# Kernel optimization log

Measured on AMD Instinct MI355X. Metric: run time of the kernel, lower is better.

Reference implementation:

```python
import jax, jax.numpy as jnp
import numpy as np

N_WAY = 5
K_SHOT = 5
SEQ = 196          # patch tokens per image (ViT-S/16 @ 224)
TEMP = 0.0510310363  # similarity temperature ~ 1/sqrt(384)
LR = 0.1
OPT_STEPS = 15


def _normalize(emb):
    # [B, S, D] -> [B*S, D], rows L2-normalized with 1e-8 floor (matches torch.max(norm, 1e-8))
    v = emb.reshape(-1, emb.shape[-1])
    n = jnp.linalg.norm(v, axis=1, keepdims=True)
    return v / jnp.maximum(n, 1e-8)


def _block_mask():
    # block_diag of (SEQ x SEQ) blocks of -100 for each of the n_way*k_shot support images
    return jnp.kron(jnp.eye(N_WAY * K_SHOT, dtype=jnp.float32),
                    jnp.ones((SEQ, SEQ), jnp.float32)) * (-100.0)


def _predict(sup, qry, v, mask):
    # sup: [n_way*k_shot, S, D], qry: [Qb, Qs, D], v: [n_way*k_shot*S]
    S = sup.shape[1]
    Qb, Qs = qry.shape[0], qry.shape[1]
    C = _normalize(sup) @ _normalize(qry).T           # [Ls, Qb*Qs] cosine sims
    if mask is not None:
        C = C + mask
    pred = C + v[:, None]
    pred = pred.reshape(N_WAY, K_SHOT * S, Qb, Qs)
    pred = pred.transpose(0, 1, 3, 2).reshape(N_WAY, K_SHOT * S * Qs, Qb)
    pred = pred / TEMP
    pred = jax.scipy.special.logsumexp(pred, axis=1)  # [n_way, Qb]
    return pred.T                                     # [Qb, n_way]


def _optimize_v(sup_key, sup_query, labels, mask):
    # online SGD on the patch-embedding importance vector v (starts at zero)
    Ls = N_WAY * K_SHOT * sup_key.shape[1]
    B = sup_query.shape[0]

    def loss(v):
        p = _predict(sup_key, sup_query, v, mask)  # [B, n_way]
        logp = jax.nn.log_softmax(p, axis=1)
        return -jnp.mean(logp[jnp.arange(B), labels])

    def step(v, _):
        return v - LR * jax.grad(loss)(v), None

    v, _ = jax.lax.scan(step, jnp.zeros((Ls,), jnp.float32), None, length=OPT_STEPS)
    return v


def setup_inputs() -> dict:
    key = jax.random.key(0)
    k1, k2, k3, k4 = jax.random.split(key, 4)
    return {
        "support_emb_key": jax.random.normal(k1, (N_WAY * K_SHOT, SEQ, 384), jnp.float32),
        "support_emb_query": jax.random.normal(k2, (N_WAY * K_SHOT, SEQ, 384), jnp.float32),
        "query_emb": jax.random.normal(k3, (75, SEQ, 384), jnp.float32),
        "support_labels": jax.random.randint(k4, (N_WAY * K_SHOT,), 0, N_WAY, dtype=jnp.int32),
    }


def reference(support_emb_key, support_emb_query, query_emb, support_labels):
    mask = _block_mask()
    v = _optimize_v(support_emb_key, support_emb_query, support_labels, mask)
    return _predict(support_emb_key, query_emb, v, None)  # [75, n_way]
```

## Files before the change

### kernel.cpp

```cpp
#include <hip/hip_runtime.h>
#include <hip/hip_bf16.h>

#define NW 5
#define KS 5
#define SEQ 196
#define DIM 384
#define NSUP 25
#define NQRY 75
#define NIMG 100
#define LSUP 4900
#define LSUP_PAD 4992
#define QROWS 208
#define BLOCK_W 980
#define OPT_STEPS 15
#define MTILES 39

static constexpr float TEMP_F = 0.0510310363f;
static constexpr float INV_T  = 1.0f / TEMP_F;
static constexpr float LR_F   = 0.1f;

typedef short v8s __attribute__((ext_vector_type(8)));
typedef float v4f __attribute__((ext_vector_type(4)));

__device__ inline unsigned short f2bf(float x) {
    unsigned int u = __float_as_uint(x);
    u += 0x7fffu + ((u >> 16) & 1u);
    return (unsigned short)(u >> 16);
}

__global__ __launch_bounds__(128) void norm_k(const float* __restrict__ src,
                                              unsigned short* __restrict__ dst) {
    int row = blockIdx.x;
    unsigned short* out = dst + (size_t)row * DIM;
    int t = threadIdx.x;
    if (row >= LSUP) {
        out[t] = 0; out[t + 128] = 0; out[t + 256] = 0;
        return;
    }
    const float* in = src + (size_t)row * DIM;
    float x0 = in[t], x1 = in[t + 128], x2 = in[t + 256];
    float s = x0 * x0 + x1 * x1 + x2 * x2;
    #pragma unroll
    for (int off = 32; off; off >>= 1) s += __shfl_down(s, off);
    __shared__ float wsum[2];
    if ((t & 63) == 0) wsum[t >> 6] = s;
    __syncthreads();
    float sc = INV_T / fmaxf(sqrtf(wsum[0] + wsum[1]), 1e-8f);
    out[t]       = f2bf(x0 * sc);
    out[t + 128] = f2bf(x1 * sc);
    out[t + 256] = f2bf(x2 * sc);
}

__global__ __launch_bounds__(128) void norm_q(const float* __restrict__ supq,
                                              const float* __restrict__ qry,
                                              unsigned short* __restrict__ dst) {
    int r = blockIdx.x;
    int img = blockIdx.y;
    unsigned short* out = dst + ((size_t)img * QROWS + r) * DIM;
    int t = threadIdx.x;
    if (r >= SEQ) {
        out[t] = 0; out[t + 128] = 0; out[t + 256] = 0;
        return;
    }
    const float* in = (img < NSUP)
        ? supq + ((size_t)img * SEQ + r) * DIM
        : qry  + ((size_t)(img - NSUP) * SEQ + r) * DIM;
    float x0 = in[t], x1 = in[t + 128], x2 = in[t + 256];
    float s = x0 * x0 + x1 * x1 + x2 * x2;
    #pragma unroll
    for (int off = 32; off; off >>= 1) s += __shfl_down(s, off);
    __shared__ float wsum[2];
    if ((t & 63) == 0) wsum[t >> 6] = s;
    __syncthreads();
    float sc = 1.0f / fmaxf(sqrtf(wsum[0] + wsum[1]), 1e-8f);
    out[t]       = f2bf(x0 * sc);
    out[t + 128] = f2bf(x1 * sc);
    out[t + 256] = f2bf(x2 * sc);
}

#define MT  128
#define NTP 208
#define NTT 13
#define KCC 64

__device__ __forceinline__ void gload16(const void* g, void* l) {
    __builtin_amdgcn_global_load_lds(
        (__attribute__((address_space(1))) void*)g,
        (__attribute__((address_space(3))) void*)l, 16, 0, 0);
}

__global__ __launch_bounds__(256, 3) void fused_expsum_mfma(
    const unsigned short* __restrict__ Kb,
    const unsigned short* __restrict__ Qall,
    float* __restrict__ Rall)
{
    __shared__ __align__(16) unsigned short Asm[MT * KCC];
    __shared__ __align__(16) unsigned short Bsm[NTP * KCC];

    int t = threadIdx.x;

    int bid = blockIdx.x;
    int xcd = bid & 7;
    int sub = bid >> 3;
    const int qq = (MTILES * NIMG) >> 3;
    const int rr = (MTILES * NIMG) & 7;
    int L = (xcd < rr ? xcd * (qq + 1) : rr * (qq + 1) + (xcd - rr) * qq) + sub;
    int img = L / MTILES;
    int m_base = (L - img * MTILES) * MT;

    const unsigned short* Qimg = Qall + (size_t)img * (QROWS * DIM);

    int wv = t >> 6;
    int l  = t & 63;
    int lo = l & 15;
    int hi = l >> 4;

    int srow = l >> 3;
    int skp  = (l & 7) ^ srow;
    const unsigned short* aSrc = Kb   + (size_t)(m_base + wv * 32 + srow) * DIM + skp * 8;
    const unsigned short* bSrc = Qimg + (size_t)srow * DIM + skp * 8;

    v4f acc0[NTT], acc1[NTT];
    #pragma unroll
    for (int n = 0; n < NTT; ++n) {
        acc0[n] = (v4f){0.f, 0.f, 0.f, 0.f};
        acc1[n] = (v4f){0.f, 0.f, 0.f, 0.f};
    }

    for (int kb = 0; kb < DIM; kb += KCC) {
        #pragma unroll
        for (int j = 0; j < 4; ++j)
            gload16(aSrc + (size_t)j * 8 * DIM + kb,
                    Asm + (wv * 32 + j * 8) * KCC);
        #pragma unroll
        for (int jj = 0; jj < 7; ++jj) {
            int j = wv + jj * 4;
            if (j < 26)
                gload16(bSrc + (size_t)j * 8 * DIM + kb,
                        Bsm + j * 8 * KCC);
        }
        __syncthreads();

        const unsigned short* Ar0 = Asm + (wv * 32 + lo) * KCC;
        const unsigned short* Br  = Bsm + lo * KCC;
        #pragma unroll
        for (int kk = 0; kk < 2; ++kk) {
            int koff = ((hi + 4 * kk) ^ (lo & 7)) * 8;
            v8s a0 = *(const v8s*)(Ar0 + koff);
            v8s a1 = *(const v8s*)(Ar0 + 16 * KCC + koff);
            #pragma unroll
            for (int n = 0; n < NTT; ++n) {
                v8s bb = *(const v8s*)(Br + n * 16 * KCC + koff);
                acc0[n] = __builtin_amdgcn_mfma_f32_16x16x32_bf16(a0, bb, acc0[n], 0, 0, 0);
                acc1[n] = __builtin_amdgcn_mfma_f32_16x16x32_bf16(a1, bb, acc1[n], 0, 0, 0);
            }
        }
        __syncthreads();
    }

    float s0[4] = {0.f, 0.f, 0.f, 0.f}, s1[4] = {0.f, 0.f, 0.f, 0.f};
    #pragma unroll
    for (int n = 0; n < NTT; ++n) {
        bool ok = (n * 16 + lo) < SEQ;
        #pragma unroll
        for (int j = 0; j < 4; ++j) {
            s0[j] += ok ? __expf(acc0[n][j]) : 0.f;
            s1[j] += ok ? __expf(acc1[n][j]) : 0.f;
        }
    }
    #pragma unroll
    for (int m = 1; m < 16; m <<= 1) {
        #pragma unroll
        for (int j = 0; j < 4; ++j) {
            s0[j] += __shfl_xor(s0[j], m);
            s1[j] += __shfl_xor(s1[j], m);
        }
    }
    if (lo == 0) {
        #pragma unroll
        for (int j = 0; j < 4; ++j) {
            int r0 = m_base + wv * 32 + hi * 4 + j;
            int r1 = r0 + 16;
            if (r0 < LSUP) {
                float o = s0[j];
                if (img < NSUP && (r0 / SEQ) == img) o = 0.f;
                Rall[(size_t)img * LSUP + r0] = o;
            }
            if (r1 < LSUP) {
                float o = s1[j];
                if (img < NSUP && (r1 / SEQ) == img) o = 0.f;
                Rall[(size_t)img * LSUP + r1] = o;
            }
        }
    }
}

__global__ __launch_bounds__(512) void opt_fused(
    const float* __restrict__ Rall,
    const int* __restrict__ labels,
    float* __restrict__ Dbufs,
    float* __restrict__ out,
    int* __restrict__ bar)
{
    __shared__ float cfs[NSUP];
    __shared__ float red[8][NSUP];
    __shared__ float esm[512];

    int blk = blockIdx.x;
    int w = blk >> 1, h = blk & 1;
    int t = threadIdx.x;
    int wave = t >> 6, lane = t & 63;
    bool act = t < 490;
    int ls = w * BLOCK_W + h * 490 + t;

    int gen = 0;
    auto gridbar = [&]() {
        __syncthreads();
        if (t == 0) {
            ++gen;
            __hip_atomic_fetch_add(bar, 1, __ATOMIC_RELEASE, __HIP_MEMORY_SCOPE_AGENT);
            while (__hip_atomic_load(bar, __ATOMIC_ACQUIRE, __HIP_MEMORY_SCOPE_AGENT) < gen * 10) {}
        }
        __syncthreads();
    };

    float Rv[NSUP];
    #pragma unroll
    for (int b = 0; b < NSUP; ++b)
        Rv[b] = act ? Rall[(size_t)b * LSUP + ls] : 0.f;

    float vv = 0.f;
    float e  = 1.f;

    {
        float part[NSUP];
        #pragma unroll
        for (int b = 0; b < NSUP; ++b) part[b] = Rv[b];
        #pragma unroll
        for (int b = 0; b < NSUP; ++b) {
            #pragma unroll
            for (int m = 32; m; m >>= 1) part[b] += __shfl_xor(part[b], m);
        }
        if (lane == 0) {
            #pragma unroll
            for (int b = 0; b < NSUP; ++b) red[wave][b] = part[b];
        }
        __syncthreads();
        if (t < NSUP) {
            float s = 0.f;
            #pragma unroll
            for (int wv2 = 0; wv2 < 8; ++wv2) s += red[wv2][t];
            atomicAdd(&Dbufs[t * 5 + w], s);
        }
    }

    for (int s = 0; s < OPT_STEPS; ++s) {
        gridbar();
        const float* Dp = Dbufs + s * 125;
        if (t < NSUP) {
            int b = t;
            float Dsum = 0.f, Dw = 1.f;
            #pragma unroll
            for (int ww = 0; ww < 5; ++ww) {
                float d = Dp[b * 5 + ww];
                Dsum += d;
                if (ww == w) Dw = d;
            }
            int y = labels[b];
            cfs[b] = ((Dw / Dsum) - (w == y ? 1.f : 0.f)) * (INV_T / 25.f) / Dw;
        }
        __syncthreads();
        float g = 0.f;
        #pragma unroll
        for (int b = 0; b < NSUP; ++b) g += cfs[b] * Rv[b];
        if (act) {
            vv -= LR_F * e * g;
            e = __expf(vv * INV_T);
        }
        __syncthreads();
        if (s + 1 < OPT_STEPS) {
            float part[NSUP];
            #pragma unroll
            for (int b = 0; b < NSUP; ++b) part[b] = e * Rv[b];
            #pragma unroll
            for (int b = 0; b < NSUP; ++b) {
                #pragma unroll
                for (int m = 32; m; m >>= 1) part[b] += __shfl_xor(part[b], m);
            }
            if (lane == 0) {
                #pragma unroll
                for (int b = 0; b < NSUP; ++b) red[wave][b] = part[b];
            }
            __syncthreads();
            if (t < NSUP) {
                float s2 = 0.f;
                #pragma unroll
                for (int wv2 = 0; wv2 < 8; ++wv2) s2 += red[wv2][t];
                atomicAdd(&Dbufs[(s + 1) * 125 + t * 5 + w], s2);
            }
        }
    }

    esm[t] = act ? e : 0.f;
    __syncthreads();
    for (int qb = wave; qb < NQRY; qb += 8) {
        const float* R = Rall + (size_t)(NSUP + qb) * LSUP + w * BLOCK_W + h * 490;
        float p = 0.f;
        for (int i = lane; i < 490; i += 64) p += esm[i] * R[i];
        #pragma unroll
        for (int m = 32; m; m >>= 1) p += __shfl_xor(p, m);
        if (lane == 0) atomicAdd(&out[qb * 5 + w], p);
    }
    gridbar();
    if (blk == 0) {
        for (int i = t; i < NQRY * NW; i += 512) out[i] = logf(out[i]);
    }
}

extern "C" void kernel_launch(void* const* d_in, const int* in_sizes, int n_in,
                              void* d_out, int out_size, void* d_ws, size_t ws_size,
                              hipStream_t stream) {
    const float* sup_key = (const float*)d_in[0];
    const float* sup_qry = (const float*)d_in[1];
    const float* qry     = (const float*)d_in[2];
    const int*   labels  = (const int*)d_in[3];
    float* out = (float*)d_out;

    char* ws = (char*)d_ws;
    size_t off = 0;
    auto take = [&](size_t bytes) {
        char* p = ws + off;
        off = (off + bytes + 255) & ~(size_t)255;
        return p;
    };
    unsigned short* Kb   = (unsigned short*)take((size_t)LSUP_PAD * DIM * 2);
    unsigned short* Qall = (unsigned short*)take((size_t)NIMG * QROWS * DIM * 2);
    float*          Rall = (float*)take((size_t)NIMG * LSUP * 4);
    float*          Dbuf = (float*)take(((size_t)(OPT_STEPS + 1) * 125 + 64) * 4);
    int*            bar  = (int*)(Dbuf + (OPT_STEPS + 1) * 125);

    hipMemsetAsync(Dbuf, 0, ((size_t)(OPT_STEPS + 1) * 125 + 64) * 4, stream);
    hipMemsetAsync(out, 0, (size_t)NQRY * NW * 4, stream);

    norm_k<<<LSUP_PAD, 128, 0, stream>>>(sup_key, Kb);
    norm_q<<<dim3(QROWS, NIMG), 128, 0, stream>>>(sup_qry, qry, Qall);

    fused_expsum_mfma<<<MTILES * NIMG, 256, 0, stream>>>(Kb, Qall, Rall);

    opt_fused<<<10, 512, 0, stream>>>(Rall, labels, Dbuf, out, bar);
}
```

Before: 256.5 us.

## Retile MFMA waves to 64x112, use wave-per-row norms, drop grid barrier

The GEMM kernel now gives each wave a 64-row by 112-column tile instead of 32x208, so each B fragment loaded from LDS feeds four MFMAs rather than two. The two column halves are then combined through shared memory before writing Rall. The norm kernels use one wave per row with a shuffle-only reduction and no __syncthreads. The optimizer kernel runs with 5 blocks of 1024 threads instead of 10. It replaces the atomic grid barrier with per-slot release stores and spin-polling on nonzero values, and the final log is computed directly without atomics. The spin on nonzero values assumes no partial sum is ever exactly zero, and the retiled GEMM uses more accumulator registers.

Result: slower. 326.8 us (+27.4%).

```diff
diff --git a/kernel.cpp b/kernel.cpp
--- a/kernel.cpp
+++ b/kernel.cpp
@@ -28,54 +28,56 @@
     return (unsigned short)(u >> 16);
 }
 
-__global__ __launch_bounds__(128) void norm_k(const float* __restrict__ src,
+__global__ __launch_bounds__(256) void norm_k(const float* __restrict__ src,
                                               unsigned short* __restrict__ dst) {
-    int row = blockIdx.x;
+    int row = blockIdx.x * 4 + (threadIdx.x >> 6);
+    int l = threadIdx.x & 63;
     unsigned short* out = dst + (size_t)row * DIM;
-    int t = threadIdx.x;
     if (row >= LSUP) {
-        out[t] = 0; out[t + 128] = 0; out[t + 256] = 0;
+        #pragma unroll
+        for (int k = 0; k < 6; ++k) out[l + 64 * k] = 0;
         return;
     }
     const float* in = src + (size_t)row * DIM;
-    float x0 = in[t], x1 = in[t + 128], x2 = in[t + 256];
-    float s = x0 * x0 + x1 * x1 + x2 * x2;
-    #pragma unroll
-    for (int off = 32; off; off >>= 1) s += __shfl_down(s, off);
-    __shared__ float wsum[2];
-    if ((t & 63) == 0) wsum[t >> 6] = s;
-    __syncthreads();
-    float sc = INV_T / fmaxf(sqrtf(wsum[0] + wsum[1]), 1e-8f);
-    out[t]       = f2bf(x0 * sc);
-    out[t + 128] = f2bf(x1 * sc);
-    out[t + 256] = f2bf(x2 * sc);
-}
-
-__global__ __launch_bounds__(128) void norm_q(const float* __restrict__ supq,
+    float x[6];
+    #pragma unroll
+    for (int k = 0; k < 6; ++k) x[k] = in[l + 64 * k];
+    float s = 0.f;
+    #pragma unroll
+    for (int k = 0; k < 6; ++k) s += x[k] * x[k];
+    #pragma unroll
+    for (int m = 1; m < 64; m <<= 1) s += __shfl_xor(s, m);
+    float sc = INV_T / fmaxf(sqrtf(s), 1e-8f);
+    #pragma unroll
+    for (int k = 0; k < 6; ++k) out[l + 64 * k] = f2bf(x[k] * sc);
+}
+
+__global__ __launch_bounds__(256) void norm_q(const float* __restrict__ supq,
                                               const float* __restrict__ qry,
                                               unsigned short* __restrict__ dst) {
-    int r = blockIdx.x;
+    int r = blockIdx.x * 4 + (threadIdx.x >> 6);
     int img = blockIdx.y;
+    int l = threadIdx.x & 63;
     unsigned short* out = dst + ((size_t)img * QROWS + r) * DIM;
-    int t = threadIdx.x;
     if (r >= SEQ) {
-        out[t] = 0; out[t + 128] = 0; out[t + 256] = 0;
+        #pragma unroll
+        for (int k = 0; k < 6; ++k) out[l + 64 * k] = 0;
         return;
     }
     const float* in = (img < NSUP)
         ? supq + ((size_t)img * SEQ + r) * DIM
         : qry  + ((size_t)(img - NSUP) * SEQ + r) * DIM;
-    float x0 = in[t], x1 = in[t + 128], x2 = in[t + 256];
-    float s = x0 * x0 + x1 * x1 + x2 * x2;
-    #pragma unroll
-    for (int off = 32; off; off >>= 1) s += __shfl_down(s, off);
-    __shared__ float wsum[2];
-    if ((t & 63) == 0) wsum[t >> 6] = s;
-    __syncthreads();
-    float sc = 1.0f / fmaxf(sqrtf(wsum[0] + wsum[1]), 1e-8f);
-    out[t]       = f2bf(x0 * sc);
-    out[t + 128] = f2bf(x1 * sc);
-    out[t + 256] = f2bf(x2 * sc);
+    float x[6];
+    #pragma unroll
+    for (int k = 0; k < 6; ++k) x[k] = in[l + 64 * k];
+    float s = 0.f;
+    #pragma unroll
+    for (int k = 0; k < 6; ++k) s += x[k] * x[k];
+    #pragma unroll
+    for (int m = 1; m < 64; m <<= 1) s += __shfl_xor(s, m);
+    float sc = 1.0f / fmaxf(sqrtf(s), 1e-8f);
+    #pragma unroll
+    for (int k = 0; k < 6; ++k) out[l + 64 * k] = f2bf(x[k] * sc);
 }
 
 #define MT  128
@@ -114,18 +116,20 @@
     int l  = t & 63;
     int lo = l & 15;
     int hi = l >> 4;
+    int mh = (wv >> 1) * 64;
+    int nh = wv & 1;
 
     int srow = l >> 3;
     int skp  = (l & 7) ^ srow;
     const unsigned short* aSrc = Kb   + (size_t)(m_base + wv * 32 + srow) * DIM + skp * 8;
     const unsigned short* bSrc = Qimg + (size_t)srow * DIM + skp * 8;
 
-    v4f acc0[NTT], acc1[NTT];
-    #pragma unroll
-    for (int n = 0; n < NTT; ++n) {
-        acc0[n] = (v4f){0.f, 0.f, 0.f, 0.f};
-        acc1[n] = (v4f){0.f, 0.f, 0.f, 0.f};
-    }
+    v4f acc[4][7];
+    #pragma unroll
+    for (int m = 0; m < 4; ++m)
+        #pragma unroll
+        for (int n = 0; n < 7; ++n)
+            acc[m][n] = (v4f){0.f, 0.f, 0.f, 0.f};
 
     for (int kb = 0; kb < DIM; kb += KCC) {
         #pragma unroll
@@ -141,101 +145,103 @@
         }
         __syncthreads();
 
-        const unsigned short* Ar0 = Asm + (wv * 32 + lo) * KCC;
-        const unsigned short* Br  = Bsm + lo * KCC;
+        const unsigned short* Ar = Asm + (mh + lo) * KCC;
+        const unsigned short* Br = Bsm + (nh * 112 + lo) * KCC;
         #pragma unroll
         for (int kk = 0; kk < 2; ++kk) {
             int koff = ((hi + 4 * kk) ^ (lo & 7)) * 8;
-            v8s a0 = *(const v8s*)(Ar0 + koff);
-            v8s a1 = *(const v8s*)(Ar0 + 16 * KCC + koff);
-            #pragma unroll
-            for (int n = 0; n < NTT; ++n) {
-                v8s bb = *(const v8s*)(Br + n * 16 * KCC + koff);
-                acc0[n] = __builtin_amdgcn_mfma_f32_16x16x32_bf16(a0, bb, acc0[n], 0, 0, 0);
-                acc1[n] = __builtin_amdgcn_mfma_f32_16x16x32_bf16(a1, bb, acc1[n], 0, 0, 0);
+            v8s a0 = *(const v8s*)(Ar + koff);
+            v8s a1 = *(const v8s*)(Ar + 16 * KCC + koff);
+            v8s a2 = *(const v8s*)(Ar + 32 * KCC + koff);
+            v8s a3 = *(const v8s*)(Ar + 48 * KCC + koff);
+            #pragma unroll
+            for (int n = 0; n < 7; ++n) {
+                if (nh == 0 || n < 6) {
+                    v8s bb = *(const v8s*)(Br + n * 16 * KCC + koff);
+                    acc[0][n] = __builtin_amdgcn_mfma_f32_16x16x32_bf16(a0, bb, acc[0][n], 0, 0, 0);
+                    acc[1][n] = __builtin_amdgcn_mfma_f32_16x16x32_bf16(a1, bb, acc[1][n], 0, 0, 0);
+                    acc[2][n] = __builtin_amdgcn_mfma_f32_16x16x32_bf16(a2, bb, acc[2][n], 0, 0, 0);
+                    acc[3][n] = __builtin_amdgcn_mfma_f32_16x16x32_bf16(a3, bb, acc[3][n], 0, 0, 0);
+                }
             }
         }
         __syncthreads();
     }
 
-    float s0[4] = {0.f, 0.f, 0.f, 0.f}, s1[4] = {0.f, 0.f, 0.f, 0.f};
-    #pragma unroll
-    for (int n = 0; n < NTT; ++n) {
-        bool ok = (n * 16 + lo) < SEQ;
-        #pragma unroll
-        for (int j = 0; j < 4; ++j) {
-            s0[j] += ok ? __expf(acc0[n][j]) : 0.f;
-            s1[j] += ok ? __expf(acc1[n][j]) : 0.f;
-        }
-    }
-    #pragma unroll
-    for (int m = 1; m < 16; m <<= 1) {
-        #pragma unroll
-        for (int j = 0; j < 4; ++j) {
-            s0[j] += __shfl_xor(s0[j], m);
-            s1[j] += __shfl_xor(s1[j], m);
-        }
-    }
+    float s[4][4];
+    #pragma unroll
+    for (int m = 0; m < 4; ++m)
+        #pragma unroll
+        for (int j = 0; j < 4; ++j) s[m][j] = 0.f;
+    #pragma unroll
+    for (int n = 0; n < 7; ++n) {
+        if (nh == 0 || n < 6) {
+            bool ok = ((nh * 7 + n) * 16 + lo) < SEQ;
+            #pragma unroll
+            for (int m = 0; m < 4; ++m)
+                #pragma unroll
+                for (int j = 0; j < 4; ++j)
+                    s[m][j] += ok ? __expf(acc[m][n][j]) : 0.f;
+        }
+    }
+    #pragma unroll
+    for (int mm = 1; mm < 16; mm <<= 1) {
+        #pragma unroll
+        for (int m = 0; m < 4; ++m)
+            #pragma unroll
+            for (int j = 0; j < 4; ++j)
+                s[m][j] += __shfl_xor(s[m][j], mm);
+    }
+    float* rp = (float*)Asm;
     if (lo == 0) {
         #pragma unroll
-        for (int j = 0; j < 4; ++j) {
-            int r0 = m_base + wv * 32 + hi * 4 + j;
-            int r1 = r0 + 16;
-            if (r0 < LSUP) {
-                float o = s0[j];
-                if (img < NSUP && (r0 / SEQ) == img) o = 0.f;
-                Rall[(size_t)img * LSUP + r0] = o;
-            }
-            if (r1 < LSUP) {
-                float o = s1[j];
-                if (img < NSUP && (r1 / SEQ) == img) o = 0.f;
-                Rall[(size_t)img * LSUP + r1] = o;
-            }
-        }
-    }
-}
-
-__global__ __launch_bounds__(512) void opt_fused(
+        for (int m = 0; m < 4; ++m)
+            #pragma unroll
+            for (int j = 0; j < 4; ++j)
+                rp[nh * 128 + mh + m * 16 + hi * 4 + j] = s[m][j];
+    }
+    __syncthreads();
+    if (t < MT) {
+        int gr = m_base + t;
+        if (gr < LSUP) {
+            float o = rp[t] + rp[128 + t];
+            if (img < NSUP && (gr / SEQ) == img) o = 0.f;
+            Rall[(size_t)img * LSUP + gr] = o;
+        }
+    }
+}
+
+__global__ __launch_bounds__(1024) void opt_fused(
     const float* __restrict__ Rall,
     const int* __restrict__ labels,
     float* __restrict__ Dbufs,
-    float* __restrict__ out,
-    int* __restrict__ bar)
+    float* __restrict__ out)
 {
+    __shared__ float Dsm[125];
     __shared__ float cfs[NSUP];
-    __shared__ float red[8][NSUP];
-    __shared__ float esm[512];
-
-    int blk = blockIdx.x;
-    int w = blk >> 1, h = blk & 1;
+    __shared__ float red[16][NSUP];
+    __shared__ float esm[BLOCK_W];
+    __shared__ int lsm[NSUP];
+
+    int w = blockIdx.x;
     int t = threadIdx.x;
     int wave = t >> 6, lane = t & 63;
-    bool act = t < 490;
-    int ls = w * BLOCK_W + h * 490 + t;
-
-    int gen = 0;
-    auto gridbar = [&]() {
-        __syncthreads();
-        if (t == 0) {
-            ++gen;
-            __hip_atomic_fetch_add(bar, 1, __ATOMIC_RELEASE, __HIP_MEMORY_SCOPE_AGENT);
-            while (__hip_atomic_load(bar, __ATOMIC_ACQUIRE, __HIP_MEMORY_SCOPE_AGENT) < gen * 10) {}
-        }
-        __syncthreads();
-    };
+    bool act = t < BLOCK_W;
+    int ls = w * BLOCK_W + t;
 
     float Rv[NSUP];
     #pragma unroll
     for (int b = 0; b < NSUP; ++b)
         Rv[b] = act ? Rall[(size_t)b * LSUP + ls] : 0.f;
+    if (t < NSUP) lsm[t] = labels[t];
 
     float vv = 0.f;
     float e  = 1.f;
 
-    {
+    auto pushD = [&](int step) {
         float part[NSUP];
         #pragma unroll
-        for (int b = 0; b < NSUP; ++b) part[b] = Rv[b];
+        for (int b = 0; b < NSUP; ++b) part[b] = e * Rv[b];
         #pragma unroll
         for (int b = 0; b < NSUP; ++b) {
             #pragma unroll
@@ -249,25 +255,34 @@
         if (t < NSUP) {
             float s = 0.f;
             #pragma unroll
-            for (int wv2 = 0; wv2 < 8; ++wv2) s += red[wv2][t];
-            atomicAdd(&Dbufs[t * 5 + w], s);
-        }
-    }
+            for (int k = 0; k < 16; ++k) s += red[k][t];
+            __hip_atomic_store(&Dbufs[step * 125 + t * 5 + w], s,
+                               __ATOMIC_RELEASE, __HIP_MEMORY_SCOPE_AGENT);
+        }
+    };
+
+    pushD(0);
 
     for (int s = 0; s < OPT_STEPS; ++s) {
-        gridbar();
-        const float* Dp = Dbufs + s * 125;
+        if (t < 125) {
+            float dv;
+            do {
+                dv = __hip_atomic_load(&Dbufs[s * 125 + t],
+                                       __ATOMIC_ACQUIRE, __HIP_MEMORY_SCOPE_AGENT);
+            } while (dv == 0.f);
+            Dsm[t] = dv;
+        }
+        __syncthreads();
         if (t < NSUP) {
             int b = t;
             float Dsum = 0.f, Dw = 1.f;
             #pragma unroll
             for (int ww = 0; ww < 5; ++ww) {
-                float d = Dp[b * 5 + ww];
+                float d = Dsm[b * 5 + ww];
                 Dsum += d;
                 if (ww == w) Dw = d;
             }
-            int y = labels[b];
-            cfs[b] = ((Dw / Dsum) - (w == y ? 1.f : 0.f)) * (INV_T / 25.f) / Dw;
+            cfs[b] = ((Dw / Dsum) - (w == lsm[b] ? 1.f : 0.f)) * (INV_T / 25.f) / Dw;
         }
         __syncthreads();
         float g = 0.f;
@@ -277,43 +292,22 @@
             vv -= LR_F * e * g;
             e = __expf(vv * INV_T);
         }
-        __syncthreads();
         if (s + 1 < OPT_STEPS) {
-            float part[NSUP];
-            #pragma unroll
-            for (int b = 0; b < NSUP; ++b) part[b] = e * Rv[b];
-            #pragma unroll
-            for (int b = 0; b < NSUP; ++b) {
-                #pragma unroll
-                for (int m = 32; m; m >>= 1) part[b] += __shfl_xor(part[b], m);
-            }
-            if (lane == 0) {
-                #pragma unroll
-                for (int b = 0; b < NSUP; ++b) red[wave][b] = part[b];
-            }
             __syncthreads();
-            if (t < NSUP) {
-                float s2 = 0.f;
-                #pragma unroll
-                for (int wv2 = 0; wv2 < 8; ++wv2) s2 += red[wv2][t];
-                atomicAdd(&Dbufs[(s + 1) * 125 + t * 5 + w], s2);
-            }
-        }
-    }
-
-    esm[t] = act ? e : 0.f;
+            pushD(s + 1);
+        }
+    }
+
+    esm[0] = 0.f;
+    if (act) esm[t] = e;
     __syncthreads();
-    for (int qb = wave; qb < NQRY; qb += 8) {
-        const float* R = Rall + (size_t)(NSUP + qb) * LSUP + w * BLOCK_W + h * 490;
+    for (int qb = wave; qb < NQRY; qb += 16) {
+        const float* R = Rall + (size_t)(NSUP + qb) * LSUP + w * BLOCK_W;
         float p = 0.f;
-        for (int i = lane; i < 490; i += 64) p += esm[i] * R[i];
+        for (int i = lane; i < BLOCK_W; i += 64) p += esm[i] * R[i];
         #pragma unroll
         for (int m = 32; m; m >>= 1) p += __shfl_xor(p, m);
-        if (lane == 0) atomicAdd(&out[qb * 5 + w], p);
-    }
-    gridbar();
-    if (blk == 0) {
-        for (int i = t; i < NQRY * NW; i += 512) out[i] = logf(out[i]);
+        if (lane == 0) out[qb * 5 + w] = logf(p);
     }
 }
 
@@ -336,16 +330,14 @@
     unsigned short* Kb   = (unsigned short*)take((size_t)LSUP_PAD * DIM * 2);
     unsigned short* Qall = (unsigned short*)take((size_t)NIMG * QROWS * DIM * 2);
     float*          Rall = (float*)take((size_t)NIMG * LSUP * 4);
-    float*          Dbuf = (float*)take(((size_t)(OPT_STEPS + 1) * 125 + 64) * 4);
-    int*            bar  = (int*)(Dbuf + (OPT_STEPS + 1) * 125);
-
-    hipMemsetAsync(Dbuf, 0, ((size_t)(OPT_STEPS + 1) * 125 + 64) * 4, stream);
-    hipMemsetAsync(out, 0, (size_t)NQRY * NW * 4, stream);
-
-    norm_k<<<LSUP_PAD, 128, 0, stream>>>(sup_key, Kb);
-    norm_q<<<dim3(QROWS, NIMG), 128, 0, stream>>>(sup_qry, qry, Qall);
+    float*          Dbuf = (float*)take((size_t)(OPT_STEPS + 1) * 125 * 4);
+
+    hipMemsetAsync(Dbuf, 0, (size_t)(OPT_STEPS + 1) * 125 * 4, stream);
+
+    norm_k<<<LSUP_PAD / 4, 256, 0, stream>>>(sup_key, Kb);
+    norm_q<<<dim3(QROWS / 4, NIMG), 256, 0, stream>>>(sup_qry, qry, Qall);
 
     fused_expsum_mfma<<<MTILES * NIMG, 256, 0, stream>>>(Kb, Qall, Rall);
 
-    opt_fused<<<10, 512, 0, stream>>>(Rall, labels, Dbuf, out, bar);
-}
+    opt_fused<<<NW, 1024, 0, stream>>>(Rall, labels, Dbuf, out);
+}
```
